# Optimization experiments

Hardware: AMD Instinct MI355X
Metric: run time of the kernel (lower is better)

The kernel has to match this reference:

```python
import jax, jax.numpy as jnp
import numpy as np

B, T, D_MODEL, N_HEADS, N_KV = 2, 2048, 1024, 16, 4
HEAD = D_MODEL // N_HEADS  # 64
NEG_INF = -1e9


def sine_table(features, length):
    # standard RoPE frequency table: theta_i = 10000^(2i/d)
    fraction = jnp.arange(0, features, 2, dtype=jnp.float32) / features
    timescale = 10000.0 ** fraction  # (features/2,)
    sinusoid = jnp.arange(length, dtype=jnp.float32)[:, None] / timescale[None, :]
    sinusoid = jnp.concatenate([sinusoid, sinusoid], axis=-1)  # (L, features)
    return jnp.sin(sinusoid), jnp.cos(sinusoid)


def rotate_half(x):
    x1, x2 = jnp.split(x, 2, axis=-1)
    return jnp.concatenate([-x2, x1], axis=-1)


def apply_rope(x, sin, cos):
    # x: (B, H, T, D); sin/cos: (L, D)
    t = x.shape[-2]
    return x * cos[:t][None, None] + rotate_half(x) * sin[:t][None, None]


def setup_inputs() -> dict:
    key = jax.random.key(0)
    k1, k2, k3, k4 = jax.random.split(key, 4)
    return {
        'q': jax.random.normal(k1, (B, T, D_MODEL), dtype=jnp.float32),
        'k': jax.random.normal(k2, (B, T, N_KV * HEAD), dtype=jnp.float32),
        'v': jax.random.normal(k3, (B, T, N_KV * HEAD), dtype=jnp.float32),
        'w_out': jax.random.normal(k4, (D_MODEL, D_MODEL), dtype=jnp.float32) * 0.02,
    }


def reference(q, k, v, w_out):
    Bq, Tq, C = q.shape
    head = C // N_HEADS
    # split heads: q -> (B, n_heads, T, head); k/v -> (B, n_kv, T, head)
    qh = q.reshape(Bq, Tq, N_HEADS, head).transpose(0, 2, 1, 3)
    kh = k.reshape(Bq, Tq, N_KV, head).transpose(0, 2, 1, 3)
    vh = v.reshape(Bq, Tq, N_KV, head).transpose(0, 2, 1, 3)
    # inline RoPE on q and k
    sin, cos = sine_table(head, Tq)
    qh = apply_rope(qh, sin, cos)
    kh = apply_rope(kh, sin, cos)
    # GQA repeat of kv heads to match q heads
    rep = N_HEADS // N_KV
    kh = jnp.repeat(kh, rep, axis=1)
    vh = jnp.repeat(vh, rep, axis=1)
    # manual scaled-dot-product attention with causal masking (full T^2 logits)
    logits = jnp.einsum('bhqd,bhkd->bhqk', qh, kh) / jnp.sqrt(jnp.float32(head))
    causal = jnp.tril(jnp.ones((Tq, Tq), dtype=jnp.float32))
    logits = jnp.where(causal == 0, NEG_INF, logits)
    attn = jax.nn.softmax(logits, axis=-1)
    out = jnp.einsum('bhqk,bhkd->bhqd', attn, vh)
    out = out.transpose(0, 2, 1, 3).reshape(Bq, Tq, C)
    return out @ w_out
```

## Files before the change

kernel.cpp:

```cpp
#include <hip/hip_runtime.h>
#include <math.h>

#define T_SEQ 2048
#define NH    16
#define NKV   4

typedef __attribute__((ext_vector_type(8))) _Float16 f16x8;
typedef __attribute__((ext_vector_type(4))) _Float16 f16x4;
typedef __attribute__((ext_vector_type(4))) float    f32x4;

__global__ __launch_bounds__(256) void prep_kernel(const float* __restrict__ k,
                                                   const float* __restrict__ v,
                                                   const float* __restrict__ w,
                                                   float2* __restrict__ tb,
                                                   _Float16* __restrict__ Kr,
                                                   _Float16* __restrict__ Vt,
                                                   _Float16* __restrict__ Wt)
{
    __shared__ _Float16 L[64 * 72];
    const int bx = blockIdx.x;
    if (bx < 256) {
        int idx = bx * 256 + threadIdx.x;
        int i = idx & 31, t = idx >> 5;
        float inv = __expf((float)i * (-9.210340371976184f / 32.0f));
        float ang = (float)t * inv;
        tb[idx] = make_float2(cosf(ang), sinf(ang));
    } else if (bx < 2304) {
        int idx = (bx - 256) * 256 + threadIdx.x;
        int i   = idx & 31;
        int t   = (idx >> 5) & 2047;
        int bk  = idx >> 16;
        float inv = __expf((float)i * (-9.210340371976184f / 32.0f));
        float ang = (float)t * inv;
        float sn = sinf(ang), cs = cosf(ang);
        const float* src = k + ((size_t)(bk >> 2) * T_SEQ + t) * 256 + (bk & 3) * 64 + i;
        float x1 = src[0], x2 = src[32];
        _Float16* dst = Kr + ((size_t)bk * T_SEQ + t) * 64 + i;
        dst[0]  = (_Float16)(x1 * cs - x2 * sn);
        dst[32] = (_Float16)(x2 * cs + x1 * sn);
    } else if (bx < 2560) {
        const int id = bx - 2304;
        const int t0 = (id & 31) * 64, bk = id >> 5;
        const int b = bk >> 2, kh = bk & 3;
        const int rr = threadIdx.x >> 2, pp = threadIdx.x & 3;
        const float* src = v + ((size_t)(b * T_SEQ + t0 + rr)) * 256 + kh * 64 + pp * 16;
        f32x4 s0 = *(const f32x4*)(src), s1 = *(const f32x4*)(src + 4);
        f32x4 s2 = *(const f32x4*)(src + 8), s3 = *(const f32x4*)(src + 12);
        _Float16* lp = &L[rr * 72 + pp * 16];
        #pragma unroll
        for (int j = 0; j < 4; ++j) { lp[j] = (_Float16)s0[j]; lp[4+j] = (_Float16)s1[j];
                                      lp[8+j] = (_Float16)s2[j]; lp[12+j] = (_Float16)s3[j]; }
        __syncthreads();
        f16x8 w0, w1;
        #pragma unroll
        for (int j = 0; j < 8; ++j) w0[j] = L[(pp * 16 + j) * 72 + rr];
        #pragma unroll
        for (int j = 0; j < 8; ++j) w1[j] = L[(pp * 16 + 8 + j) * 72 + rr];
        _Float16* dst = Vt + ((size_t)bk * 64 + rr) * T_SEQ + t0 + pp * 16;
        *(f16x8*)dst = w0; *(f16x8*)(dst + 8) = w1;
    } else {
        const int id = bx - 2560;
        const int k0 = (id & 15) * 64, n0 = (id >> 4) * 64;
        const int rr = threadIdx.x >> 2, pp = threadIdx.x & 3;
        const float* src = w + (size_t)(k0 + rr) * 1024 + n0 + pp * 16;
        f32x4 s0 = *(const f32x4*)(src), s1 = *(const f32x4*)(src + 4);
        f32x4 s2 = *(const f32x4*)(src + 8), s3 = *(const f32x4*)(src + 12);
        _Float16* lp = &L[rr * 72 + pp * 16];
        #pragma unroll
        for (int j = 0; j < 4; ++j) { lp[j] = (_Float16)s0[j]; lp[4+j] = (_Float16)s1[j];
                                      lp[8+j] = (_Float16)s2[j]; lp[12+j] = (_Float16)s3[j]; }
        __syncthreads();
        f16x8 w0, w1;
        #pragma unroll
        for (int j = 0; j < 8; ++j) w0[j] = L[(pp * 16 + j) * 72 + rr];
        #pragma unroll
        for (int j = 0; j < 8; ++j) w1[j] = L[(pp * 16 + 8 + j) * 72 + rr];
        _Float16* dst = Wt + (size_t)(n0 + rr) * 1024 + k0 + pp * 16;
        *(f16x8*)dst = w0; *(f16x8*)(dst + 8) = w1;
    }
}


__global__ __launch_bounds__(256) void attn_kernel(const float* __restrict__ q,
                                                   const float2* __restrict__ tb,
                                                   const _Float16* __restrict__ Kr,
                                                   const _Float16* __restrict__ Vt,
                                                   _Float16* __restrict__ AO)
{
    __shared__ _Float16 smem[16384];

    const int wid  = threadIdx.x >> 6;
    const int lane = threadIdx.x & 63;
    const int bh = blockIdx.x & 31;
    const int p  = blockIdx.x >> 5;
    const int qb0 = p, qb1 = 31 - p;
    const int b = bh >> 4, h = bh & 15;
    const int kh = h >> 2;
    const int bkh = b * NKV + kh;
    const int g = lane >> 4, r = lane & 15;

    const int srow   = wid * 16 + (lane >> 3);
    const int schunk = lane & 7;
    const _Float16* kgbase = Kr + (size_t)bkh * T_SEQ * 64;
    const _Float16* vgbase = Vt + (size_t)bkh * 64 * T_SEQ;
    const int kd0 = srow * 64 + ((schunk ^ (srow & 7)) * 8);
    const int kd1 = kd0 + 8 * 64;

    f16x8 stK0, stK1, stV0, stV1;
    {
        const _Float16* kg = kgbase + (size_t)srow * 64 + schunk * 8;
        stK0 = *(const f16x8*)(kg);
        stK1 = *(const f16x8*)(kg + 8 * 64);
        const _Float16* vg = vgbase + (size_t)srow * T_SEQ + schunk * 8;
        stV0 = *(const f16x8*)(vg);
        stV1 = *(const f16x8*)(vg + 8 * T_SEQ);
    }

    f16x8 qa[2][2];
    #pragma unroll
    for (int tl = 0; tl < 2; ++tl) {
        const int t = (tl ? qb1 : qb0) * 64 + wid * 16 + r;
        const float* qs = q + ((size_t)b * T_SEQ + t) * 1024 + h * 64 + 8 * g;
        const float2* tp = tb + t * 32 + 8 * g;
        #pragma unroll
        for (int j = 0; j < 8; ++j) {
            float x0 = qs[j], x1 = qs[32 + j];
            float2 cs = tp[j];
            qa[tl][0][j] = (_Float16)((x0 * cs.x - x1 * cs.y) * 0.125f);
            qa[tl][1][j] = (_Float16)((x1 * cs.x + x0 * cs.y) * 0.125f);
        }
    }

    *(f16x8*)(&smem[kd0])        = stK0;
    *(f16x8*)(&smem[kd1])        = stK1;
    *(f16x8*)(&smem[8192 + kd0]) = stV0;
    *(f16x8*)(&smem[8192 + kd1]) = stV1;
    __syncthreads();

    f32x4 o[2][4];
    f32x4 o4[2];
    #pragma unroll
    for (int tl = 0; tl < 2; ++tl) {
        #pragma unroll
        for (int db = 0; db < 4; ++db) o[tl][db] = (f32x4){0.f,0.f,0.f,0.f};
        o4[tl] = (f32x4){0.f,0.f,0.f,0.f};
    }
    const f16x4 onesf = {(_Float16)1.f, (_Float16)1.f, (_Float16)1.f, (_Float16)1.f};
    float mrun[2] = {-INFINITY, -INFINITY};
    int cur = 0;

    for (int kvb = 0; kvb <= qb1; ++kvb) {
        const bool hasNext = (kvb < qb1);
        if (hasNext) {
            const int nb = (kvb + 1) * 64;
            const _Float16* kg = kgbase + (size_t)(nb + srow) * 64 + schunk * 8;
            stK0 = *(const f16x8*)(kg);
            stK1 = *(const f16x8*)(kg + 8 * 64);
            const _Float16* vg = vgbase + (size_t)srow * T_SEQ + nb + schunk * 8;
            stV0 = *(const f16x8*)(vg);
            stV1 = *(const f16x8*)(vg + 8 * T_SEQ);
        }
        const bool act0 = (kvb <= qb0);
        const _Float16* ks = smem + cur * 4096;
        const _Float16* vs = smem + 8192 + cur * 4096;

        f32x4 stt[2][4];
        __builtin_amdgcn_s_setprio(1);
        #pragma unroll
        for (int kt = 0; kt < 4; ++kt) {
            f16x8 ka0 = *(const f16x8*)(ks + (kt*16 + r) * 64 + ((g       ^ (r & 7)) * 8));
            f16x8 ka1 = *(const f16x8*)(ks + (kt*16 + r) * 64 + (((4 + g) ^ (r & 7)) * 8));
            f32x4 s1 = {0.f,0.f,0.f,0.f};
            s1 = __builtin_amdgcn_mfma_f32_16x16x32_f16(ka0, qa[1][0], s1, 0, 0, 0);
            s1 = __builtin_amdgcn_mfma_f32_16x16x32_f16(ka1, qa[1][1], s1, 0, 0, 0);
            stt[1][kt] = s1;
            if (act0) {
                f32x4 s0 = {0.f,0.f,0.f,0.f};
                s0 = __builtin_amdgcn_mfma_f32_16x16x32_f16(ka0, qa[0][0], s0, 0, 0, 0);
                s0 = __builtin_amdgcn_mfma_f32_16x16x32_f16(ka1, qa[0][1], s0, 0, 0, 0);
                stt[0][kt] = s0;
            }
        }
        __builtin_amdgcn_s_setprio(0);

        if (kvb == qb0) {
            #pragma unroll
            for (int kt = 0; kt < 4; ++kt)
                #pragma unroll
                for (int j = 0; j < 4; ++j)
                    if (kt*16 + 4*g + j > wid*16 + r) stt[0][kt][j] = -1e9f;
        }
        if (kvb == qb1) {
            #pragma unroll
            for (int kt = 0; kt < 4; ++kt)
                #pragma unroll
                for (int j = 0; j < 4; ++j)
                    if (kt*16 + 4*g + j > wid*16 + r) stt[1][kt][j] = -1e9f;
        }

        f16x4 pf[2][4];
        #pragma unroll
        for (int tl = 0; tl < 2; ++tl) {
            if (tl == 0 && !act0) continue;
            float a0 = fmaxf(fmaxf(stt[tl][0][0], stt[tl][0][1]),
                             fmaxf(stt[tl][0][2], stt[tl][0][3]));
            float a1 = fmaxf(fmaxf(stt[tl][1][0], stt[tl][1][1]),
                             fmaxf(stt[tl][1][2], stt[tl][1][3]));
            float a2 = fmaxf(fmaxf(stt[tl][2][0], stt[tl][2][1]),
                             fmaxf(stt[tl][2][2], stt[tl][2][3]));
            float a3 = fmaxf(fmaxf(stt[tl][3][0], stt[tl][3][1]),
                             fmaxf(stt[tl][3][2], stt[tl][3][3]));
            float pmL = fmaxf(fmaxf(a0, a1), fmaxf(a2, a3));
            if (!__all(pmL <= mrun[tl] + 8.0f)) {
                float pm = fmaxf(pmL, __shfl_xor(pmL, 16));
                pm = fmaxf(pm, __shfl_xor(pm, 32));
                float mn   = fmaxf(mrun[tl], pm);
                float corr = __expf(mrun[tl] - mn);
                mrun[tl]   = mn;
                f32x4 cf = { __shfl(corr, 4*g + 0), __shfl(corr, 4*g + 1),
                             __shfl(corr, 4*g + 2), __shfl(corr, 4*g + 3) };
                o[tl][0] *= cf; o[tl][1] *= cf; o[tl][2] *= cf; o[tl][3] *= cf;
                o4[tl]   *= cf;
            }
            #pragma unroll
            for (int kt = 0; kt < 4; ++kt) {
                float p0 = __expf(stt[tl][kt][0] - mrun[tl]);
                float p1 = __expf(stt[tl][kt][1] - mrun[tl]);
                float p2 = __expf(stt[tl][kt][2] - mrun[tl]);
                float p3 = __expf(stt[tl][kt][3] - mrun[tl]);
                pf[tl][kt] = (f16x4){(_Float16)p0, (_Float16)p1,
                                     (_Float16)p2, (_Float16)p3};
            }
        }

        __builtin_amdgcn_s_setprio(1);
        #pragma unroll
        for (int kt = 0; kt < 4; ++kt) {
            const int vc = ((2*kt + (g >> 1)) ^ (r & 7)) * 8 + (g & 1) * 4;
            f16x4 v0 = *(const f16x4*)(vs + (0*16 + r) * 64 + vc);
            f16x4 v1 = *(const f16x4*)(vs + (1*16 + r) * 64 + vc);
            f16x4 v2 = *(const f16x4*)(vs + (2*16 + r) * 64 + vc);
            f16x4 v3 = *(const f16x4*)(vs + (3*16 + r) * 64 + vc);
            o[1][0] = __builtin_amdgcn_mfma_f32_16x16x16f16(pf[1][kt], v0, o[1][0], 0, 0, 0);
            o[1][1] = __builtin_amdgcn_mfma_f32_16x16x16f16(pf[1][kt], v1, o[1][1], 0, 0, 0);
            o[1][2] = __builtin_amdgcn_mfma_f32_16x16x16f16(pf[1][kt], v2, o[1][2], 0, 0, 0);
            o[1][3] = __builtin_amdgcn_mfma_f32_16x16x16f16(pf[1][kt], v3, o[1][3], 0, 0, 0);
            o4[1]   = __builtin_amdgcn_mfma_f32_16x16x16f16(pf[1][kt], onesf, o4[1], 0, 0, 0);
            if (act0) {
                o[0][0] = __builtin_amdgcn_mfma_f32_16x16x16f16(pf[0][kt], v0, o[0][0], 0, 0, 0);
                o[0][1] = __builtin_amdgcn_mfma_f32_16x16x16f16(pf[0][kt], v1, o[0][1], 0, 0, 0);
                o[0][2] = __builtin_amdgcn_mfma_f32_16x16x16f16(pf[0][kt], v2, o[0][2], 0, 0, 0);
                o[0][3] = __builtin_amdgcn_mfma_f32_16x16x16f16(pf[0][kt], v3, o[0][3], 0, 0, 0);
                o4[0]   = __builtin_amdgcn_mfma_f32_16x16x16f16(pf[0][kt], onesf, o4[0], 0, 0, 0);
            }
        }
        __builtin_amdgcn_s_setprio(0);

        if (hasNext) {
            _Float16* kw = smem + (cur ^ 1) * 4096;
            _Float16* vw = smem + 8192 + (cur ^ 1) * 4096;
            *(f16x8*)(&kw[kd0]) = stK0;
            *(f16x8*)(&kw[kd1]) = stK1;
            *(f16x8*)(&vw[kd0]) = stV0;
            *(f16x8*)(&vw[kd1]) = stV1;
            cur ^= 1;
        }
        __syncthreads();
    }

    #pragma unroll
    for (int tl = 0; tl < 2; ++tl) {
        f32x4 li;
        #pragma unroll
        for (int j = 0; j < 4; ++j) li[j] = 1.0f / o4[tl][j];
        _Float16* Os = smem + tl * 4608;
        #pragma unroll
        for (int db = 0; db < 4; ++db) {
            f32x4 ov = o[tl][db] * li;
            #pragma unroll
            for (int j = 0; j < 4; ++j)
                Os[(wid*16 + 4*g + j) * 72 + db*16 + r] = (_Float16)ov[j];
        }
    }
    __syncthreads();
    {
        const int row = threadIdx.x >> 2, part = threadIdx.x & 3;
        #pragma unroll
        for (int tl = 0; tl < 2; ++tl) {
            const int qb = tl ? qb1 : qb0;
            const _Float16* src = smem + tl * 4608 + row * 72 + part * 16;
            _Float16* dst = AO + ((size_t)b * T_SEQ + qb * 64 + row) * 1024 + h * 64 + part * 16;
            *(f16x8*)dst       = *(const f16x8*)src;
            *(f16x8*)(dst + 8) = *(const f16x8*)(src + 8);
        }
    }
}


#define AST 40
__global__ __launch_bounds__(256) void gemm_kernel(const _Float16* __restrict__ A,
                                                   const _Float16* __restrict__ Bt,
                                                   float* __restrict__ C)
{
    __shared__ _Float16 As[2][128 * AST];
    __shared__ _Float16 Bs[2][64 * AST];
    const int tid  = threadIdx.x;
    const int by   = blockIdx.x & 31;
    const int bx   = blockIdx.x >> 5;
    const int lane = tid & 63;
    const int wid  = tid >> 6;
    const int g = lane >> 4, r = lane & 15;
    const int wm = wid >> 1, wn = wid & 1;

    f32x4 acc[4][2];
    #pragma unroll
    for (int i = 0; i < 4; ++i)
        #pragma unroll
        for (int j = 0; j < 2; ++j) acc[i][j] = (f32x4){0.f,0.f,0.f,0.f};

    const int c0 = tid, c1 = tid + 256;
    const size_t a0off = (size_t)(by*128 + (c0 >> 2)) * 1024 + (c0 & 3) * 8;
    const size_t a1off = (size_t)(by*128 + (c1 >> 2)) * 1024 + (c1 & 3) * 8;
    const size_t b0off = (size_t)(bx*64  + (c0 >> 2)) * 1024 + (c0 & 3) * 8;
    const int ad0 = (c0 >> 2) * AST + (c0 & 3) * 8;
    const int ad1 = (c1 >> 2) * AST + (c1 & 3) * 8;

    f16x8 a0 = *(const f16x8*)(A  + a0off);
    f16x8 a1 = *(const f16x8*)(A  + a1off);
    f16x8 b0 = *(const f16x8*)(Bt + b0off);
    *(f16x8*)(&As[0][ad0]) = a0;
    *(f16x8*)(&As[0][ad1]) = a1;
    *(f16x8*)(&Bs[0][ad0]) = b0;
    __syncthreads();
    int cur = 0;

    for (int kt = 0; kt < 32; ++kt) {
        if (kt < 31) {
            a0 = *(const f16x8*)(A  + a0off + (kt+1) * 32);
            a1 = *(const f16x8*)(A  + a1off + (kt+1) * 32);
            b0 = *(const f16x8*)(Bt + b0off + (kt+1) * 32);
        }
        f16x8 af[4], bfv[2];
        #pragma unroll
        for (int mi = 0; mi < 4; ++mi)
            af[mi] = *(const f16x8*)(&As[cur][(wm*64 + mi*16 + r) * AST + 8 * g]);
        #pragma unroll
        for (int ni = 0; ni < 2; ++ni)
            bfv[ni] = *(const f16x8*)(&Bs[cur][(wn*32 + ni*16 + r) * AST + 8 * g]);
        __builtin_amdgcn_s_setprio(1);
        #pragma unroll
        for (int mi = 0; mi < 4; ++mi)
            #pragma unroll
            for (int ni = 0; ni < 2; ++ni)
                acc[mi][ni] = __builtin_amdgcn_mfma_f32_16x16x32_f16(
                                  af[mi], bfv[ni], acc[mi][ni], 0, 0, 0);
        __builtin_amdgcn_s_setprio(0);
        if (kt < 31) {
            *(f16x8*)(&As[cur ^ 1][ad0]) = a0;
            *(f16x8*)(&As[cur ^ 1][ad1]) = a1;
            *(f16x8*)(&Bs[cur ^ 1][ad0]) = b0;
            cur ^= 1;
        }
        __syncthreads();
    }
    #pragma unroll
    for (int mi = 0; mi < 4; ++mi)
        #pragma unroll
        for (int ni = 0; ni < 2; ++ni)
            #pragma unroll
            for (int j = 0; j < 4; ++j)
                C[(size_t)(by*128 + wm*64 + mi*16 + 4*g + j) * 1024
                  + bx*64 + wn*32 + ni*16 + r] = acc[mi][ni][j];
}


extern "C" void kernel_launch(void* const* d_in, const int* in_sizes, int n_in,
                              void* d_out, int out_size, void* d_ws, size_t ws_size,
                              hipStream_t stream) {
    const float* q = (const float*)d_in[0];
    const float* k = (const float*)d_in[1];
    const float* v = (const float*)d_in[2];
    const float* w = (const float*)d_in[3];
    float* out = (float*)d_out;

    char* ws = (char*)d_ws;
    float2*   tb = (float2*)(ws);
    _Float16* Kr = (_Float16*)(ws + ((size_t)1 << 20));
    _Float16* Vt = (_Float16*)(ws + ((size_t)3 << 20));
    _Float16* Wt = (_Float16*)(ws + ((size_t)5 << 20));
    _Float16* AO = (_Float16*)(ws + ((size_t)7 << 20));

    hipLaunchKernelGGL(prep_kernel,  dim3(2816), dim3(256), 0, stream, k, v, w, tb, Kr, Vt, Wt);
    hipLaunchKernelGGL(attn_kernel,  dim3(512),  dim3(256), 0, stream, q, tb, Kr, Vt, AO);
    hipLaunchKernelGGL(gemm_kernel,  dim3(512),  dim3(256), 0, stream, AO, Wt, out);
}
```

Before: 76.72 us.

## Use exp2 softmax with folded log2e scale, pack conversions, reorder blocks, shrink prep grid

Folds log2(e) into the query scale so softmax can use the native exp2 instruction instead of __expf, and packs the fp16 probability conversions with cvt_pkrtz. The K-rope prep now reuses one sin/cos computation across all 8 batch-kv heads per thread, cutting the prep grid from 2816 to 1024 blocks. Attention block indices are remapped so the q-block pairing order changes, which may improve tail balance. Round-toward-zero conversion slightly changes rounding of the probabilities.

Result: faster. 74.46 us (-2.9%).

```diff
diff --git a/kernel.cpp b/kernel.cpp
--- a/kernel.cpp
+++ b/kernel.cpp
@@ -5,9 +5,18 @@
 #define NH    16
 #define NKV   4
 
-typedef __attribute__((ext_vector_type(8))) _Float16 f16x8;
-typedef __attribute__((ext_vector_type(4))) _Float16 f16x4;
-typedef __attribute__((ext_vector_type(4))) float    f32x4;
+typedef __attribute__((ext_vector_type(8)))  _Float16 f16x8;
+typedef __attribute__((ext_vector_type(4)))  _Float16 f16x4;
+typedef __attribute__((ext_vector_type(2)))  __fp16   fp16x2b;
+typedef __attribute__((ext_vector_type(4)))  float    f32x4;
+
+#if __has_builtin(__builtin_amdgcn_exp2f)
+#define EXP2F(x) __builtin_amdgcn_exp2f(x)
+#else
+#define EXP2F(x) exp2f(x)
+#endif
+
+#define QSCALE 0.18033688011112042f
 
 __global__ __launch_bounds__(256) void prep_kernel(const float* __restrict__ k,
                                                    const float* __restrict__ v,
@@ -25,21 +34,23 @@
         float inv = __expf((float)i * (-9.210340371976184f / 32.0f));
         float ang = (float)t * inv;
         tb[idx] = make_float2(cosf(ang), sinf(ang));
-    } else if (bx < 2304) {
+    } else if (bx < 512) {
         int idx = (bx - 256) * 256 + threadIdx.x;
         int i   = idx & 31;
-        int t   = (idx >> 5) & 2047;
-        int bk  = idx >> 16;
+        int t   = idx >> 5;
         float inv = __expf((float)i * (-9.210340371976184f / 32.0f));
         float ang = (float)t * inv;
         float sn = sinf(ang), cs = cosf(ang);
-        const float* src = k + ((size_t)(bk >> 2) * T_SEQ + t) * 256 + (bk & 3) * 64 + i;
-        float x1 = src[0], x2 = src[32];
-        _Float16* dst = Kr + ((size_t)bk * T_SEQ + t) * 64 + i;
-        dst[0]  = (_Float16)(x1 * cs - x2 * sn);
-        dst[32] = (_Float16)(x2 * cs + x1 * sn);
-    } else if (bx < 2560) {
-        const int id = bx - 2304;
+        #pragma unroll
+        for (int bk = 0; bk < 8; ++bk) {
+            const float* src = k + ((size_t)(bk >> 2) * T_SEQ + t) * 256 + (bk & 3) * 64 + i;
+            float x1 = src[0], x2 = src[32];
+            _Float16* dst = Kr + ((size_t)bk * T_SEQ + t) * 64 + i;
+            dst[0]  = (_Float16)(x1 * cs - x2 * sn);
+            dst[32] = (_Float16)(x2 * cs + x1 * sn);
+        }
+    } else if (bx < 768) {
+        const int id = bx - 512;
         const int t0 = (id & 31) * 64, bk = id >> 5;
         const int b = bk >> 2, kh = bk & 3;
         const int rr = threadIdx.x >> 2, pp = threadIdx.x & 3;
@@ -59,7 +70,7 @@
         _Float16* dst = Vt + ((size_t)bk * 64 + rr) * T_SEQ + t0 + pp * 16;
         *(f16x8*)dst = w0; *(f16x8*)(dst + 8) = w1;
     } else {
-        const int id = bx - 2560;
+        const int id = bx - 768;
         const int k0 = (id & 15) * 64, n0 = (id >> 4) * 64;
         const int rr = threadIdx.x >> 2, pp = threadIdx.x & 3;
         const float* src = w + (size_t)(k0 + rr) * 1024 + n0 + pp * 16;
@@ -92,7 +103,8 @@
     const int wid  = threadIdx.x >> 6;
     const int lane = threadIdx.x & 63;
     const int bh = blockIdx.x & 31;
-    const int p  = blockIdx.x >> 5;
+    const int pp = blockIdx.x >> 5;
+    const int p  = (pp < 8) ? pp : (23 - pp);
     const int qb0 = p, qb1 = 31 - p;
     const int b = bh >> 4, h = bh & 15;
     const int kh = h >> 2;
@@ -126,8 +138,8 @@
         for (int j = 0; j < 8; ++j) {
             float x0 = qs[j], x1 = qs[32 + j];
             float2 cs = tp[j];
-            qa[tl][0][j] = (_Float16)((x0 * cs.x - x1 * cs.y) * 0.125f);
-            qa[tl][1][j] = (_Float16)((x1 * cs.x + x0 * cs.y) * 0.125f);
+            qa[tl][0][j] = (_Float16)((x0 * cs.x - x1 * cs.y) * QSCALE);
+            qa[tl][1][j] = (_Float16)((x1 * cs.x + x0 * cs.y) * QSCALE);
         }
     }
 
@@ -215,7 +227,7 @@
                 float pm = fmaxf(pmL, __shfl_xor(pmL, 16));
                 pm = fmaxf(pm, __shfl_xor(pm, 32));
                 float mn   = fmaxf(mrun[tl], pm);
-                float corr = __expf(mrun[tl] - mn);
+                float corr = EXP2F(mrun[tl] - mn);
                 mrun[tl]   = mn;
                 f32x4 cf = { __shfl(corr, 4*g + 0), __shfl(corr, 4*g + 1),
                              __shfl(corr, 4*g + 2), __shfl(corr, 4*g + 3) };
@@ -224,12 +236,16 @@
             }
             #pragma unroll
             for (int kt = 0; kt < 4; ++kt) {
-                float p0 = __expf(stt[tl][kt][0] - mrun[tl]);
-                float p1 = __expf(stt[tl][kt][1] - mrun[tl]);
-                float p2 = __expf(stt[tl][kt][2] - mrun[tl]);
-                float p3 = __expf(stt[tl][kt][3] - mrun[tl]);
-                pf[tl][kt] = (f16x4){(_Float16)p0, (_Float16)p1,
-                                     (_Float16)p2, (_Float16)p3};
+                float p0 = EXP2F(stt[tl][kt][0] - mrun[tl]);
+                float p1 = EXP2F(stt[tl][kt][1] - mrun[tl]);
+                float p2 = EXP2F(stt[tl][kt][2] - mrun[tl]);
+                float p3 = EXP2F(stt[tl][kt][3] - mrun[tl]);
+                union { unsigned u[2]; f16x4 v; } pk;
+                union { fp16x2b hh; unsigned u; } c0, c1;
+                c0.hh = __builtin_amdgcn_cvt_pkrtz(p0, p1);
+                c1.hh = __builtin_amdgcn_cvt_pkrtz(p2, p3);
+                pk.u[0] = c0.u; pk.u[1] = c1.u;
+                pf[tl][kt] = pk.v;
             }
         }
 
@@ -390,7 +406,7 @@
     _Float16* Wt = (_Float16*)(ws + ((size_t)5 << 20));
     _Float16* AO = (_Float16*)(ws + ((size_t)7 << 20));
 
-    hipLaunchKernelGGL(prep_kernel,  dim3(2816), dim3(256), 0, stream, k, v, w, tb, Kr, Vt, Wt);
+    hipLaunchKernelGGL(prep_kernel,  dim3(1024), dim3(256), 0, stream, k, v, w, tb, Kr, Vt, Wt);
     hipLaunchKernelGGL(attn_kernel,  dim3(512),  dim3(256), 0, stream, q, tb, Kr, Vt, AO);
     hipLaunchKernelGGL(gemm_kernel,  dim3(512),  dim3(256), 0, stream, AO, Wt, out);
 }
```
